# Kernel tuning notes

Measured on AMD Instinct MI355X. Metric: run time of the kernel, lower is better.

The kernel has to match this reference:

```python
import jax, jax.numpy as jnp
import numpy as np

B, F, D, H, E, K = 4, 2048, 1024, 2048, 8, 2  # batch, frames, dim, expert hidden, n_experts, top_k


def setup_inputs() -> dict:
    key = jax.random.key(0)
    ks = jax.random.split(key, 9)
    sc = lambda k, shape, fan_in: (jax.random.normal(k, shape, jnp.float32) * (fan_in ** -0.5))
    return {
        "x": jax.random.normal(ks[0], (B, F, D), jnp.float32),
        # router: Linear(D,D) -> SiLU -> Linear(D,E)
        "rw1": sc(ks[1], (D, D), D),
        "rb1": jnp.zeros((D,), jnp.float32),
        "rw2": sc(ks[2], (D, E), D),
        "rb2": jnp.zeros((E,), jnp.float32),
        # experts: E x (Linear(D,H) -> SiLU -> Linear(H,D))
        "ew1": sc(ks[3], (E, D, H), D),
        "eb1": jnp.zeros((E, H), jnp.float32),
        "ew2": sc(ks[4], (E, H, D), H),
        "eb2": jnp.zeros((E, D), jnp.float32),
    }


def reference(x, rw1, rb1, rw2, rb2, ew1, eb1, ew2, eb2):
    b, f, d = x.shape
    t = x.reshape(b * f, d)                                   # [T, D]
    # router (eval mode: no topk noise)
    logits = jax.nn.silu(t @ rw1 + rb1) @ rw2 + rb2            # [T, E]
    vals, idx = jax.lax.top_k(logits, K)                       # [T, K]
    rows = jnp.arange(t.shape[0])[:, None]
    masked = jnp.full_like(logits, -jnp.inf).at[rows, idx].set(vals)
    w = jax.nn.softmax(masked, axis=1)                         # [T, E], nonzero only on top-k
    # dense per-expert FFN, then weighted combine (residual: y starts as x)
    eh = jax.nn.silu(jnp.einsum('td,edh->teh', t, ew1) + eb1[None])   # [T, E, H]
    eo = jnp.einsum('teh,ehd->ted', eh, ew2) + eb2[None]              # [T, E, D]
    y = t + jnp.einsum('te,ted->td', w, eo)
    return y.reshape(b, f, d)
```

## Files before the change

kernel.cpp:

```cpp
#include <hip/hip_runtime.h>
#include <hip/hip_bf16.h>
#include <cstdint>
#include <cstddef>

#define T_TOK 8192
#define DDIM  1024
#define HDIM  2048
#define NEXP  8
#define TOPK  2
#define KAUG  (3 * DDIM)

typedef short bf16x8 __attribute__((ext_vector_type(8)));
typedef float f32x4  __attribute__((ext_vector_type(4)));

__device__ __forceinline__ unsigned short f2bf(float f) {
  union { float f; unsigned u; } v; v.f = f;
  unsigned r = v.u + 0x7FFFu + ((v.u >> 16) & 1u);
  return (unsigned short)(r >> 16);
}
__device__ __forceinline__ float bf2f(unsigned short h) {
  union { unsigned u; float f; } v; v.u = ((unsigned)h) << 16;
  return v.f;
}
__device__ __forceinline__ float silu_fast(float v) {
  return v / (1.0f + __expf(-v));
}
__device__ __forceinline__ float silu_precise(float v) {
  return v / (1.0f + expf(-v));
}

__device__ __forceinline__ void gload16(const unsigned short* g, unsigned short* l) {
  __builtin_amdgcn_global_load_lds(
      (const __attribute__((address_space(1))) unsigned int*)g,
      (__attribute__((address_space(3))) unsigned int*)l,
      16, 0, 0);
}

__global__ void split_x_kernel(const float* __restrict__ in,
                               unsigned short* __restrict__ xaug, int n4) {
  int i = blockIdx.x * blockDim.x + threadIdx.x;
  if (i >= n4) return;
  float4 v = ((const float4*)in)[i];
  int t = i / (DDIM / 4);
  int kc = (i % (DDIM / 4)) * 4;
  float f[4] = {v.x, v.y, v.z, v.w};
  ushort4 hi, lo;
  unsigned short h[4], l[4];
#pragma unroll
  for (int j = 0; j < 4; j++) {
    h[j] = f2bf(f[j]);
    l[j] = f2bf(f[j] - bf2f(h[j]));
  }
  hi.x = h[0]; hi.y = h[1]; hi.z = h[2]; hi.w = h[3];
  lo.x = l[0]; lo.y = l[1]; lo.z = l[2]; lo.w = l[3];
  *(ushort4*)&xaug[(size_t)t * KAUG + kc] = hi;
  *(ushort4*)&xaug[(size_t)t * KAUG + DDIM + kc] = hi;
  *(ushort4*)&xaug[(size_t)t * KAUG + 2 * DDIM + kc] = lo;
}

__global__ __launch_bounds__(256) void split_w_kernel(
    const float* __restrict__ in, unsigned short* __restrict__ waug) {
  __shared__ float tile[32][33];
  int c0 = blockIdx.x * 32, r0 = blockIdx.y * 32;
  int tx = threadIdx.x & 31, ty = threadIdx.x >> 5;
#pragma unroll
  for (int i = 0; i < 32; i += 8)
    tile[ty + i][tx] = in[(size_t)(r0 + ty + i) * DDIM + (c0 + tx)];
  __syncthreads();
#pragma unroll
  for (int i = 0; i < 32; i += 8) {
    float v = tile[tx][ty + i];
    unsigned short h = f2bf(v);
    unsigned short l = f2bf(v - bf2f(h));
    int n = c0 + ty + i, k = r0 + tx;
    waug[(size_t)n * KAUG + k] = h;
    waug[(size_t)n * KAUG + DDIM + k] = l;
    waug[(size_t)n * KAUG + 2 * DDIM + k] = h;
  }
}

__global__ __launch_bounds__(256) void transpose_conv_kernel(
    const float* __restrict__ in, unsigned short* __restrict__ out, int R, int C) {
  __shared__ float tile[32][33];
  const int z = blockIdx.z;
  const float* src = in + (size_t)z * R * C;
  unsigned short* dst = out + (size_t)z * R * C;
  int c0 = blockIdx.x * 32, r0 = blockIdx.y * 32;
  int tx = threadIdx.x & 31, ty = threadIdx.x >> 5;
#pragma unroll
  for (int i = 0; i < 32; i += 8)
    tile[ty + i][tx] = src[(size_t)(r0 + ty + i) * C + (c0 + tx)];
  __syncthreads();
#pragma unroll
  for (int i = 0; i < 32; i += 8)
    dst[(size_t)(c0 + ty + i) * R + (r0 + tx)] = f2bf(tile[tx][ty + i]);
}

__global__ void zero_small_kernel(int* __restrict__ counts, int* __restrict__ cursors) {
  int i = threadIdx.x;
  if (i < NEXP) { counts[i] = 0; cursors[i] = 0; }
}

template <int EPI>
__global__ __launch_bounds__(512, 2) void gemm_mfma4(
    const unsigned short* __restrict__ Abase,
    const unsigned short* __restrict__ Btbase,
    const float* __restrict__ bias,
    float* __restrict__ outF,
    unsigned short* __restrict__ outBf,
    const int* __restrict__ toks,
    const int* __restrict__ offs, const int* __restrict__ cnts,
    int N, int KD, int Astride, int numE, int nTiles, int mCap) {
  constexpr int BUFB = 49152;
  extern __shared__ char sm[];

  const int id = blockIdx.x;
  const int e = id % numE;
  const int r = id / numE;
  const int n0 = (r % nTiles) * 256;
  const int mb = r / nTiles;

  int ne = T_TOK, off = 0;
  if (EPI != 0) { ne = cnts[e]; off = offs[e]; }

  const unsigned short* Bt = Btbase + (size_t)e * N * KD;
  const unsigned short* A = (EPI == 2) ? (Abase + (size_t)off * Astride) : Abase;

  const int tid = threadIdx.x;
  const int lane = tid & 63, wid = tid >> 6;
  const int l16 = lane & 15, quad = lane >> 4;
  const int wm = wid >> 2, wn = wid & 3;

  const int rStage = tid >> 3;
  const int cS8 = ((tid & 7) ^ (rStage & 7)) * 8;
  const int ldsW = wid << 10;

  const int NT = KD / 64;
  const int mStride = mCap * 128;

  const int sw = l16 & 7;
  const int cOff0 = (quad ^ sw) << 4;
  const int cOff1 = ((quad + 4) ^ sw) << 4;
  const int aFragB = (wm * 64 + l16) << 7;
  const int bFragB = 16384 + ((wn * 64 + l16) << 7);

  const unsigned short* bP[4];
#pragma unroll
  for (int p = 0; p < 4; p++)
    bP[p] = Bt + (size_t)(n0 + p * 64 + rStage) * KD + cS8;

  for (int m0 = mb * 128; m0 < ne; m0 += mStride) {
    const unsigned short* aP[2];
#pragma unroll
    for (int p = 0; p < 2; p++) {
      int row = m0 + p * 64 + rStage;
      int idx;
      if (EPI == 1) idx = toks[off + min(row, ne - 1)];
      else if (EPI == 2) idx = min(row, ne - 1);
      else idx = row;
      aP[p] = A + (size_t)idx * Astride + cS8;
    }

    f32x4 acc[4][4];
    const f32x4 zf = {0.f, 0.f, 0.f, 0.f};
#pragma unroll
    for (int mi = 0; mi < 4; mi++)
#pragma unroll
      for (int ni = 0; ni < 4; ni++) acc[mi][ni] = zf;

    auto stage = [&](int t, int b) {
      char* base = sm + b * BUFB + ldsW;
      gload16(aP[0] + t * 64, (unsigned short*)(base));
      gload16(aP[1] + t * 64, (unsigned short*)(base + 8192));
      gload16(bP[0] + t * 64, (unsigned short*)(base + 16384));
      gload16(bP[1] + t * 64, (unsigned short*)(base + 24576));
      gload16(bP[2] + t * 64, (unsigned short*)(base + 32768));
      gload16(bP[3] + t * 64, (unsigned short*)(base + 40960));
    };

    stage(0, 0);
    stage(1, 1);
    stage(2, 2);

    for (int t = 0; t < NT; ++t) {
      const char* base = sm + (t % 3) * BUFB;
      if (t + 2 < NT)      __builtin_amdgcn_s_waitcnt(0x0F70 | 12);
      else if (t + 1 < NT) __builtin_amdgcn_s_waitcnt(0x0F70 | 6);
      else                 __builtin_amdgcn_s_waitcnt(0x0F70);
      __builtin_amdgcn_s_barrier();
      __builtin_amdgcn_sched_barrier(0);

      bf16x8 av[4], bv[4];
#pragma unroll
      for (int mi = 0; mi < 4; mi++)
        av[mi] = *(const bf16x8*)(base + aFragB + (mi << 11) + cOff0);
#pragma unroll
      for (int ni = 0; ni < 4; ni++)
        bv[ni] = *(const bf16x8*)(base + bFragB + (ni << 11) + cOff0);
      __builtin_amdgcn_s_waitcnt(0xC07F);
      __builtin_amdgcn_sched_barrier(0);
      __builtin_amdgcn_s_setprio(1);
#pragma unroll
      for (int mi = 0; mi < 4; mi++)
#pragma unroll
        for (int ni = 0; ni < 4; ni++)
          acc[mi][ni] = __builtin_amdgcn_mfma_f32_16x16x32_bf16(
              av[mi], bv[ni], acc[mi][ni], 0, 0, 0);
      __builtin_amdgcn_s_setprio(0);
      __builtin_amdgcn_s_barrier();

#pragma unroll
      for (int mi = 0; mi < 4; mi++)
        av[mi] = *(const bf16x8*)(base + aFragB + (mi << 11) + cOff1);
#pragma unroll
      for (int ni = 0; ni < 4; ni++)
        bv[ni] = *(const bf16x8*)(base + bFragB + (ni << 11) + cOff1);
      __builtin_amdgcn_s_waitcnt(0xC07F);
      __builtin_amdgcn_s_barrier();
      __builtin_amdgcn_sched_barrier(0);
      if (t + 3 < NT) stage(t + 3, t % 3);
      __builtin_amdgcn_s_setprio(1);
#pragma unroll
      for (int mi = 0; mi < 4; mi++)
#pragma unroll
        for (int ni = 0; ni < 4; ni++)
          acc[mi][ni] = __builtin_amdgcn_mfma_f32_16x16x32_bf16(
              av[mi], bv[ni], acc[mi][ni], 0, 0, 0);
      __builtin_amdgcn_s_setprio(0);
    }

    float bv4[4];
#pragma unroll
    for (int ni = 0; ni < 4; ni++)
      bv4[ni] = bias[(size_t)e * N + n0 + wn * 64 + ni * 16 + l16];
#pragma unroll
    for (int mi = 0; mi < 4; mi++) {
      const int prow = m0 + wm * 64 + mi * 16 + quad * 4;
#pragma unroll
      for (int rr = 0; rr < 4; rr++) {
        const int p = prow + rr;
        if (EPI != 0 && p >= ne) continue;
#pragma unroll
        for (int ni = 0; ni < 4; ni++) {
          const int col = n0 + wn * 64 + ni * 16 + l16;
          float v = acc[mi][ni][rr] + bv4[ni];
          if (EPI == 0) {
            outF[(size_t)p * N + col] = silu_precise(v);
          } else if (EPI == 1) {
            outBf[(size_t)(off + p) * N + col] = f2bf(silu_fast(v));
          } else {
            outBf[(size_t)(off + p) * N + col] = f2bf(v);
          }
        }
      }
    }
  }
}

__global__ __launch_bounds__(256) void router2_kernel(
    const float* __restrict__ rh, const float* __restrict__ rw2,
    const float* __restrict__ rb2, float* __restrict__ logits) {
  int t = blockIdx.x * 4 + (threadIdx.x >> 6);
  int lane = threadIdx.x & 63;
  const float* row = rh + (size_t)t * DDIM;
  float acc[NEXP];
#pragma unroll
  for (int e = 0; e < NEXP; e++) acc[e] = 0.f;
  for (int k = lane; k < DDIM; k += 64) {
    float v = row[k];
    const float* w = rw2 + (size_t)k * NEXP;
#pragma unroll
    for (int e = 0; e < NEXP; e++) acc[e] += v * w[e];
  }
#pragma unroll
  for (int e = 0; e < NEXP; e++) {
#pragma unroll
    for (int off = 32; off > 0; off >>= 1) acc[e] += __shfl_xor(acc[e], off, 64);
  }
#pragma unroll
  for (int e = 0; e < NEXP; e++)
    if (lane == e) logits[(size_t)t * NEXP + e] = acc[e] + rb2[e];
}

__global__ void topk_kernel(const float* __restrict__ logits,
                            int* __restrict__ idx2, float* __restrict__ w2arr,
                            int* __restrict__ counts) {
  int t = blockIdx.x * blockDim.x + threadIdx.x;
  if (t >= T_TOK) return;
  float l[NEXP];
#pragma unroll
  for (int e = 0; e < NEXP; e++) l[e] = logits[(size_t)t * NEXP + e];
  int i1 = 0; float v1 = l[0];
#pragma unroll
  for (int e = 1; e < NEXP; e++)
    if (l[e] > v1) { v1 = l[e]; i1 = e; }
  int i2 = -1; float v2 = -3.4e38f;
#pragma unroll
  for (int e = 0; e < NEXP; e++)
    if (e != i1 && l[e] > v2) { v2 = l[e]; i2 = e; }
  float ex = expf(v2 - v1);
  float wa = 1.f / (1.f + ex);
  float wb = ex / (1.f + ex);
  idx2[t * 2] = i1; idx2[t * 2 + 1] = i2;
  w2arr[t * 2] = wa; w2arr[t * 2 + 1] = wb;
  atomicAdd(&counts[i1], 1);
  atomicAdd(&counts[i2], 1);
}

__global__ void prefix_kernel(const int* __restrict__ counts, int* __restrict__ offs) {
  if (threadIdx.x == 0 && blockIdx.x == 0) {
    int s = 0;
    for (int e = 0; e < NEXP; e++) { offs[e] = s; s += counts[e]; }
  }
}

__global__ void scatter_kernel(const int* __restrict__ idx2,
                               const int* __restrict__ offs, int* __restrict__ cursors,
                               int* __restrict__ toks, int* __restrict__ posArr) {
  int t = blockIdx.x * blockDim.x + threadIdx.x;
  if (t >= T_TOK) return;
#pragma unroll
  for (int j = 0; j < TOPK; j++) {
    int e = idx2[t * 2 + j];
    int pos = atomicAdd(&cursors[e], 1);
    int s = offs[e] + pos;
    toks[s] = t;
    posArr[t * 2 + j] = s;
  }
}

__global__ __launch_bounds__(256) void combine_kernel(
    const float* __restrict__ x, const unsigned short* __restrict__ eo,
    const int* __restrict__ posArr, const float* __restrict__ w2arr,
    float* __restrict__ y) {
  const int t = blockIdx.x;
  const int d = threadIdx.x * 4;
  const int s0 = posArr[t * 2], s1 = posArr[t * 2 + 1];
  const float w0 = w2arr[t * 2], w1 = w2arr[t * 2 + 1];
  float4 xv = *(const float4*)&x[(size_t)t * DDIM + d];
  ushort4 a = *(const ushort4*)&eo[(size_t)s0 * DDIM + d];
  ushort4 b = *(const ushort4*)&eo[(size_t)s1 * DDIM + d];
  float4 o;
  o.x = xv.x + w0 * bf2f(a.x) + w1 * bf2f(b.x);
  o.y = xv.y + w0 * bf2f(a.y) + w1 * bf2f(b.y);
  o.z = xv.z + w0 * bf2f(a.z) + w1 * bf2f(b.z);
  o.w = xv.w + w0 * bf2f(a.w) + w1 * bf2f(b.w);
  *(float4*)&y[(size_t)t * DDIM + d] = o;
}

extern "C" void kernel_launch(void* const* d_in, const int* in_sizes, int n_in,
                              void* d_out, int out_size, void* d_ws, size_t ws_size,
                              hipStream_t stream) {
  (void)in_sizes; (void)n_in; (void)out_size; (void)ws_size;
  const float* x   = (const float*)d_in[0];
  const float* rw1 = (const float*)d_in[1];
  const float* rb1 = (const float*)d_in[2];
  const float* rw2 = (const float*)d_in[3];
  const float* rb2 = (const float*)d_in[4];
  const float* ew1 = (const float*)d_in[5];
  const float* eb1 = (const float*)d_in[6];
  const float* ew2 = (const float*)d_in[7];
  const float* eb2 = (const float*)d_in[8];
  float* y = (float*)d_out;

  char* ws = (char*)d_ws;
  size_t o = 0;
  auto alloc = [&](size_t bytes) {
    size_t r = o;
    o += (bytes + 255) & ~(size_t)255;
    return r;
  };
  unsigned short* xaug  = (unsigned short*)(ws + alloc((size_t)T_TOK * KAUG * 2));
  unsigned short* waug  = (unsigned short*)(ws + alloc((size_t)DDIM * KAUG * 2));
  unsigned short* ew1t  = (unsigned short*)(ws + alloc((size_t)NEXP * HDIM * DDIM * 2));
  unsigned short* ew2t  = (unsigned short*)(ws + alloc((size_t)NEXP * DDIM * HDIM * 2));
  float*          rh    = (float*)(ws + alloc((size_t)T_TOK * DDIM * 4));
  float*          logits= (float*)(ws + alloc((size_t)T_TOK * NEXP * 4));
  int*            idx2  = (int*)(ws + alloc((size_t)T_TOK * 2 * 4));
  float*          w2    = (float*)(ws + alloc((size_t)T_TOK * 2 * 4));
  int*            toks  = (int*)(ws + alloc((size_t)T_TOK * TOPK * 4));
  int*            posArr= (int*)(ws + alloc((size_t)T_TOK * TOPK * 4));
  int*            counts= (int*)(ws + alloc(256));
  int*            cursors=(int*)(ws + alloc(256));
  int*            offs  = (int*)(ws + alloc(256));
  unsigned short* ehb   = (unsigned short*)(ws + alloc((size_t)T_TOK * TOPK * HDIM * 2));
  unsigned short* eo    = (unsigned short*)(ws + alloc((size_t)T_TOK * TOPK * DDIM * 2));

  constexpr int LDS_SZ = 3 * 49152;
  static bool s_attr = false;
  if (!s_attr) {
    (void)hipFuncSetAttribute((const void*)gemm_mfma4<0>,
                              hipFuncAttributeMaxDynamicSharedMemorySize, LDS_SZ);
    (void)hipFuncSetAttribute((const void*)gemm_mfma4<1>,
                              hipFuncAttributeMaxDynamicSharedMemorySize, LDS_SZ);
    (void)hipFuncSetAttribute((const void*)gemm_mfma4<2>,
                              hipFuncAttributeMaxDynamicSharedMemorySize, LDS_SZ);
    s_attr = true;
  }

  zero_small_kernel<<<1, 64, 0, stream>>>(counts, cursors);

  const int n4 = T_TOK * DDIM / 4;
  split_x_kernel<<<(n4 + 255) / 256, 256, 0, stream>>>(x, xaug, n4);
  split_w_kernel<<<dim3(DDIM / 32, DDIM / 32), 256, 0, stream>>>(rw1, waug);
  transpose_conv_kernel<<<dim3(HDIM / 32, DDIM / 32, NEXP), 256, 0, stream>>>(ew1, ew1t, DDIM, HDIM);
  transpose_conv_kernel<<<dim3(DDIM / 32, HDIM / 32, NEXP), 256, 0, stream>>>(ew2, ew2t, HDIM, DDIM);

  gemm_mfma4<0><<<256, 512, LDS_SZ, stream>>>(
      xaug, waug, rb1, rh, nullptr, nullptr, nullptr, nullptr,
      DDIM, KAUG, KAUG, 1, 4, 64);
  router2_kernel<<<T_TOK / 4, 256, 0, stream>>>(rh, rw2, rb2, logits);
  topk_kernel<<<T_TOK / 256, 256, 0, stream>>>(logits, idx2, w2, counts);
  prefix_kernel<<<1, 64, 0, stream>>>(counts, offs);
  scatter_kernel<<<T_TOK / 256, 256, 0, stream>>>(idx2, offs, cursors, toks, posArr);

  gemm_mfma4<1><<<8 * 8 * 16, 512, LDS_SZ, stream>>>(
      xaug, ew1t, eb1, nullptr, ehb, toks, offs, counts,
      HDIM, DDIM, KAUG, NEXP, 8, 16);
  gemm_mfma4<2><<<8 * 4 * 16, 512, LDS_SZ, stream>>>(
      ehb, ew2t, eb2, nullptr, eo, nullptr, offs, counts,
      DDIM, HDIM, HDIM, NEXP, 4, 16);
  combine_kernel<<<T_TOK, 256, 0, stream>>>(x, eo, posArr, w2, y);
}
```

Baseline: 747.6 us.

## Enlarge GEMM tile to 256x256 with double-buffered quarter-staged ping-pong pipeline

Rewrites the shared MFMA GEMM so each 512-thread block computes a 256x256 output tile instead of 128x256, doubling the per-wave accumulators to 8x4. The triple-buffered LDS pipeline becomes a double buffer, and A and B halves are staged separately between four MFMA phases so loads interleave with compute. The goal is more arithmetic per byte moved through LDS and global memory. In exchange, grids shrink (128, 256 and 256 blocks), register pressure rises, and wasted padding grows for experts whose token count is not a multiple of 256.

Result: no change. 742.0 us (-0.8%).

```diff
diff --git a/kernel.cpp b/kernel.cpp
--- a/kernel.cpp
+++ b/kernel.cpp
@@ -102,7 +102,7 @@
 }
 
 template <int EPI>
-__global__ __launch_bounds__(512, 2) void gemm_mfma4(
+__global__ __launch_bounds__(512, 2) void gemm8p(
     const unsigned short* __restrict__ Abase,
     const unsigned short* __restrict__ Btbase,
     const float* __restrict__ bias,
@@ -111,7 +111,6 @@
     const int* __restrict__ toks,
     const int* __restrict__ offs, const int* __restrict__ cnts,
     int N, int KD, int Astride, int numE, int nTiles, int mCap) {
-  constexpr int BUFB = 49152;
   extern __shared__ char sm[];
 
   const int id = blockIdx.x;
@@ -136,23 +135,23 @@
   const int ldsW = wid << 10;
 
   const int NT = KD / 64;
-  const int mStride = mCap * 128;
+  const int mStride = mCap * 256;
 
   const int sw = l16 & 7;
   const int cOff0 = (quad ^ sw) << 4;
   const int cOff1 = ((quad + 4) ^ sw) << 4;
-  const int aFragB = (wm * 64 + l16) << 7;
-  const int bFragB = 16384 + ((wn * 64 + l16) << 7);
+  const int aRowB = (wm * 128 + l16) << 7;
+  const int bRowB = (wn * 64 + l16) << 7;
 
   const unsigned short* bP[4];
 #pragma unroll
   for (int p = 0; p < 4; p++)
     bP[p] = Bt + (size_t)(n0 + p * 64 + rStage) * KD + cS8;
 
-  for (int m0 = mb * 128; m0 < ne; m0 += mStride) {
-    const unsigned short* aP[2];
-#pragma unroll
-    for (int p = 0; p < 2; p++) {
+  for (int m0 = mb * 256; m0 < ne; m0 += mStride) {
+    const unsigned short* aP[4];
+#pragma unroll
+    for (int p = 0; p < 4; p++) {
       int row = m0 + p * 64 + rStage;
       int idx;
       if (EPI == 1) idx = toks[off + min(row, ne - 1)];
@@ -161,72 +160,125 @@
       aP[p] = A + (size_t)idx * Astride + cS8;
     }
 
-    f32x4 acc[4][4];
+    auto stA0 = [&](int t) { char* b = sm + (t & 1) * 32768 + ldsW; int kb = t * 64;
+      gload16(aP[0] + kb, (unsigned short*)b);
+      gload16(aP[1] + kb, (unsigned short*)(b + 8192)); };
+    auto stA1 = [&](int t) { char* b = sm + (t & 1) * 32768 + 16384 + ldsW; int kb = t * 64;
+      gload16(aP[2] + kb, (unsigned short*)b);
+      gload16(aP[3] + kb, (unsigned short*)(b + 8192)); };
+    auto stB0 = [&](int t) { char* b = sm + 65536 + (t & 1) * 32768 + ldsW; int kb = t * 64;
+      gload16(bP[0] + kb, (unsigned short*)b);
+      gload16(bP[1] + kb, (unsigned short*)(b + 8192)); };
+    auto stB1 = [&](int t) { char* b = sm + 65536 + (t & 1) * 32768 + 16384 + ldsW; int kb = t * 64;
+      gload16(bP[2] + kb, (unsigned short*)b);
+      gload16(bP[3] + kb, (unsigned short*)(b + 8192)); };
+
+    f32x4 acc[8][4];
     const f32x4 zf = {0.f, 0.f, 0.f, 0.f};
 #pragma unroll
-    for (int mi = 0; mi < 4; mi++)
+    for (int mi = 0; mi < 8; mi++)
 #pragma unroll
       for (int ni = 0; ni < 4; ni++) acc[mi][ni] = zf;
 
-    auto stage = [&](int t, int b) {
-      char* base = sm + b * BUFB + ldsW;
-      gload16(aP[0] + t * 64, (unsigned short*)(base));
-      gload16(aP[1] + t * 64, (unsigned short*)(base + 8192));
-      gload16(bP[0] + t * 64, (unsigned short*)(base + 16384));
-      gload16(bP[1] + t * 64, (unsigned short*)(base + 24576));
-      gload16(bP[2] + t * 64, (unsigned short*)(base + 32768));
-      gload16(bP[3] + t * 64, (unsigned short*)(base + 40960));
-    };
-
-    stage(0, 0);
-    stage(1, 1);
-    stage(2, 2);
+    stA0(0); stB0(0); stA1(0); stB1(0);
+    __builtin_amdgcn_s_waitcnt(0x0F74);
+    stA0(1); stB0(1); stA1(1);
+    __builtin_amdgcn_s_waitcnt(0x0F76);
+    __builtin_amdgcn_s_barrier();
 
     for (int t = 0; t < NT; ++t) {
-      const char* base = sm + (t % 3) * BUFB;
-      if (t + 2 < NT)      __builtin_amdgcn_s_waitcnt(0x0F70 | 12);
-      else if (t + 1 < NT) __builtin_amdgcn_s_waitcnt(0x0F70 | 6);
-      else                 __builtin_amdgcn_s_waitcnt(0x0F70);
-      __builtin_amdgcn_s_barrier();
-      __builtin_amdgcn_sched_barrier(0);
-
-      bf16x8 av[4], bv[4];
-#pragma unroll
-      for (int mi = 0; mi < 4; mi++)
-        av[mi] = *(const bf16x8*)(base + aFragB + (mi << 11) + cOff0);
-#pragma unroll
-      for (int ni = 0; ni < 4; ni++)
-        bv[ni] = *(const bf16x8*)(base + bFragB + (ni << 11) + cOff0);
+      const char* bA = sm + (t & 1) * 32768;
+      const char* bB = bA + 65536;
+      bf16x8 aR[8], bR0[4], bR1[4];
+
+#pragma unroll
+      for (int mi = 0; mi < 4; mi++) {
+        aR[mi * 2]     = *(const bf16x8*)(bA + aRowB + mi * 2048 + cOff0);
+        aR[mi * 2 + 1] = *(const bf16x8*)(bA + aRowB + mi * 2048 + cOff1);
+      }
+#pragma unroll
+      for (int ni = 0; ni < 2; ni++) {
+        bR0[ni * 2]     = *(const bf16x8*)(bB + bRowB + ni * 2048 + cOff0);
+        bR0[ni * 2 + 1] = *(const bf16x8*)(bB + bRowB + ni * 2048 + cOff1);
+      }
+      if (t + 1 < NT) stB1(t + 1);
+      __builtin_amdgcn_s_waitcnt(0xC87F);
+      __builtin_amdgcn_s_barrier();
       __builtin_amdgcn_s_waitcnt(0xC07F);
       __builtin_amdgcn_sched_barrier(0);
       __builtin_amdgcn_s_setprio(1);
 #pragma unroll
       for (int mi = 0; mi < 4; mi++)
 #pragma unroll
-        for (int ni = 0; ni < 4; ni++)
+        for (int ni = 0; ni < 2; ni++) {
           acc[mi][ni] = __builtin_amdgcn_mfma_f32_16x16x32_bf16(
-              av[mi], bv[ni], acc[mi][ni], 0, 0, 0);
+              aR[mi * 2], bR0[ni * 2], acc[mi][ni], 0, 0, 0);
+          acc[mi][ni] = __builtin_amdgcn_mfma_f32_16x16x32_bf16(
+              aR[mi * 2 + 1], bR0[ni * 2 + 1], acc[mi][ni], 0, 0, 0);
+        }
       __builtin_amdgcn_s_setprio(0);
       __builtin_amdgcn_s_barrier();
 
 #pragma unroll
+      for (int ni = 0; ni < 2; ni++) {
+        bR1[ni * 2]     = *(const bf16x8*)(bB + bRowB + (ni + 2) * 2048 + cOff0);
+        bR1[ni * 2 + 1] = *(const bf16x8*)(bB + bRowB + (ni + 2) * 2048 + cOff1);
+      }
+      __builtin_amdgcn_s_barrier();
+      __builtin_amdgcn_s_waitcnt(0xC07F);
+      __builtin_amdgcn_sched_barrier(0);
+      __builtin_amdgcn_s_setprio(1);
+#pragma unroll
       for (int mi = 0; mi < 4; mi++)
-        av[mi] = *(const bf16x8*)(base + aFragB + (mi << 11) + cOff1);
-#pragma unroll
-      for (int ni = 0; ni < 4; ni++)
-        bv[ni] = *(const bf16x8*)(base + bFragB + (ni << 11) + cOff1);
+#pragma unroll
+        for (int ni = 0; ni < 2; ni++) {
+          acc[mi][ni + 2] = __builtin_amdgcn_mfma_f32_16x16x32_bf16(
+              aR[mi * 2], bR1[ni * 2], acc[mi][ni + 2], 0, 0, 0);
+          acc[mi][ni + 2] = __builtin_amdgcn_mfma_f32_16x16x32_bf16(
+              aR[mi * 2 + 1], bR1[ni * 2 + 1], acc[mi][ni + 2], 0, 0, 0);
+        }
+      __builtin_amdgcn_s_setprio(0);
+      __builtin_amdgcn_s_barrier();
+
+#pragma unroll
+      for (int mi = 0; mi < 4; mi++) {
+        aR[mi * 2]     = *(const bf16x8*)(bA + aRowB + (mi + 4) * 2048 + cOff0);
+        aR[mi * 2 + 1] = *(const bf16x8*)(bA + aRowB + (mi + 4) * 2048 + cOff1);
+      }
+      if (t + 2 < NT) stB0(t + 2);
+      __builtin_amdgcn_s_barrier();
       __builtin_amdgcn_s_waitcnt(0xC07F);
-      __builtin_amdgcn_s_barrier();
       __builtin_amdgcn_sched_barrier(0);
-      if (t + 3 < NT) stage(t + 3, t % 3);
       __builtin_amdgcn_s_setprio(1);
 #pragma unroll
       for (int mi = 0; mi < 4; mi++)
 #pragma unroll
-        for (int ni = 0; ni < 4; ni++)
-          acc[mi][ni] = __builtin_amdgcn_mfma_f32_16x16x32_bf16(
-              av[mi], bv[ni], acc[mi][ni], 0, 0, 0);
+        for (int ni = 0; ni < 2; ni++) {
+          acc[mi + 4][ni + 2] = __builtin_amdgcn_mfma_f32_16x16x32_bf16(
+              aR[mi * 2], bR1[ni * 2], acc[mi + 4][ni + 2], 0, 0, 0);
+          acc[mi + 4][ni + 2] = __builtin_amdgcn_mfma_f32_16x16x32_bf16(
+              aR[mi * 2 + 1], bR1[ni * 2 + 1], acc[mi + 4][ni + 2], 0, 0, 0);
+        }
       __builtin_amdgcn_s_setprio(0);
+      __builtin_amdgcn_s_barrier();
+
+      if (t + 2 < NT) { stA0(t + 2); stA1(t + 2); }
+      __builtin_amdgcn_s_barrier();
+      __builtin_amdgcn_sched_barrier(0);
+      __builtin_amdgcn_s_setprio(1);
+#pragma unroll
+      for (int mi = 0; mi < 4; mi++)
+#pragma unroll
+        for (int ni = 0; ni < 2; ni++) {
+          acc[mi + 4][ni] = __builtin_amdgcn_mfma_f32_16x16x32_bf16(
+              aR[mi * 2], bR0[ni * 2], acc[mi + 4][ni], 0, 0, 0);
+          acc[mi + 4][ni] = __builtin_amdgcn_mfma_f32_16x16x32_bf16(
+              aR[mi * 2 + 1], bR0[ni * 2 + 1], acc[mi + 4][ni], 0, 0, 0);
+        }
+      __builtin_amdgcn_s_setprio(0);
+      if (t + 2 < NT)      __builtin_amdgcn_s_waitcnt(0x0F76);
+      else if (t + 1 < NT) __builtin_amdgcn_s_waitcnt(0x0F70);
+      __builtin_amdgcn_s_barrier();
     }
 
     float bv4[4];
@@ -234,8 +286,8 @@
     for (int ni = 0; ni < 4; ni++)
       bv4[ni] = bias[(size_t)e * N + n0 + wn * 64 + ni * 16 + l16];
 #pragma unroll
-    for (int mi = 0; mi < 4; mi++) {
-      const int prow = m0 + wm * 64 + mi * 16 + quad * 4;
+    for (int mi = 0; mi < 8; mi++) {
+      const int prow = m0 + wm * 128 + mi * 16 + quad * 4;
 #pragma unroll
       for (int rr = 0; rr < 4; rr++) {
         const int p = prow + rr;
@@ -386,14 +438,14 @@
   unsigned short* ehb   = (unsigned short*)(ws + alloc((size_t)T_TOK * TOPK * HDIM * 2));
   unsigned short* eo    = (unsigned short*)(ws + alloc((size_t)T_TOK * TOPK * DDIM * 2));
 
-  constexpr int LDS_SZ = 3 * 49152;
+  constexpr int LDS_SZ = 131072;
   static bool s_attr = false;
   if (!s_attr) {
-    (void)hipFuncSetAttribute((const void*)gemm_mfma4<0>,
+    (void)hipFuncSetAttribute((const void*)gemm8p<0>,
                               hipFuncAttributeMaxDynamicSharedMemorySize, LDS_SZ);
-    (void)hipFuncSetAttribute((const void*)gemm_mfma4<1>,
+    (void)hipFuncSetAttribute((const void*)gemm8p<1>,
                               hipFuncAttributeMaxDynamicSharedMemorySize, LDS_SZ);
-    (void)hipFuncSetAttribute((const void*)gemm_mfma4<2>,
+    (void)hipFuncSetAttribute((const void*)gemm8p<2>,
                               hipFuncAttributeMaxDynamicSharedMemorySize, LDS_SZ);
     s_attr = true;
   }
@@ -406,19 +458,19 @@
   transpose_conv_kernel<<<dim3(HDIM / 32, DDIM / 32, NEXP), 256, 0, stream>>>(ew1, ew1t, DDIM, HDIM);
   transpose_conv_kernel<<<dim3(DDIM / 32, HDIM / 32, NEXP), 256, 0, stream>>>(ew2, ew2t, HDIM, DDIM);
 
-  gemm_mfma4<0><<<256, 512, LDS_SZ, stream>>>(
+  gemm8p<0><<<128, 512, LDS_SZ, stream>>>(
       xaug, waug, rb1, rh, nullptr, nullptr, nullptr, nullptr,
-      DDIM, KAUG, KAUG, 1, 4, 64);
+      DDIM, KAUG, KAUG, 1, 4, 32);
   router2_kernel<<<T_TOK / 4, 256, 0, stream>>>(rh, rw2, rb2, logits);
   topk_kernel<<<T_TOK / 256, 256, 0, stream>>>(logits, idx2, w2, counts);
   prefix_kernel<<<1, 64, 0, stream>>>(counts, offs);
   scatter_kernel<<<T_TOK / 256, 256, 0, stream>>>(idx2, offs, cursors, toks, posArr);
 
-  gemm_mfma4<1><<<8 * 8 * 16, 512, LDS_SZ, stream>>>(
+  gemm8p<1><<<8 * 8 * 4, 512, LDS_SZ, stream>>>(
       xaug, ew1t, eb1, nullptr, ehb, toks, offs, counts,
-      HDIM, DDIM, KAUG, NEXP, 8, 16);
-  gemm_mfma4<2><<<8 * 4 * 16, 512, LDS_SZ, stream>>>(
+      HDIM, DDIM, KAUG, NEXP, 8, 4);
+  gemm8p<2><<<8 * 4 * 8, 512, LDS_SZ, stream>>>(
       ehb, ew2t, eb2, nullptr, eo, nullptr, offs, counts,
-      DDIM, HDIM, HDIM, NEXP, 4, 16);
+      DDIM, HDIM, HDIM, NEXP, 4, 8);
   combine_kernel<<<T_TOK, 256, 0, stream>>>(x, eo, posArr, w2, y);
 }
```

## Shrink GEMM tiles to 128x128 with 256 threads and double buffering

Applied to the files above, without the earlier changes.

Replaces the 512-thread, 128x256-tile GEMM with a 256-thread, 128x128-tile version. The LDS pipeline drops from three stages to two (64 KB instead of 144 KB), and the next stage is prefetched at the top of each k-step. Grids double in size to cover the narrower N tiles. The aim is higher occupancy and more blocks per CU. The cost is less operand reuse per tile and a shallower prefetch that may expose global-load latency.

After: 694.1 us. -7.2%, faster.

```diff
diff --git a/kernel.cpp b/kernel.cpp
--- a/kernel.cpp
+++ b/kernel.cpp
@@ -102,7 +102,7 @@
 }
 
 template <int EPI>
-__global__ __launch_bounds__(512, 2) void gemm_mfma4(
+__global__ __launch_bounds__(256) void gemm_s(
     const unsigned short* __restrict__ Abase,
     const unsigned short* __restrict__ Btbase,
     const float* __restrict__ bias,
@@ -111,13 +111,12 @@
     const int* __restrict__ toks,
     const int* __restrict__ offs, const int* __restrict__ cnts,
     int N, int KD, int Astride, int numE, int nTiles, int mCap) {
-  constexpr int BUFB = 49152;
   extern __shared__ char sm[];
 
   const int id = blockIdx.x;
   const int e = id % numE;
   const int r = id / numE;
-  const int n0 = (r % nTiles) * 256;
+  const int n0 = (r % nTiles) * 128;
   const int mb = r / nTiles;
 
   int ne = T_TOK, off = 0;
@@ -129,7 +128,7 @@
   const int tid = threadIdx.x;
   const int lane = tid & 63, wid = tid >> 6;
   const int l16 = lane & 15, quad = lane >> 4;
-  const int wm = wid >> 2, wn = wid & 3;
+  const int wm = wid >> 1, wn = wid & 1;
 
   const int rStage = tid >> 3;
   const int cS8 = ((tid & 7) ^ (rStage & 7)) * 8;
@@ -141,19 +140,19 @@
   const int sw = l16 & 7;
   const int cOff0 = (quad ^ sw) << 4;
   const int cOff1 = ((quad + 4) ^ sw) << 4;
-  const int aFragB = (wm * 64 + l16) << 7;
-  const int bFragB = 16384 + ((wn * 64 + l16) << 7);
+  const int aRowB = (wm * 64 + l16) << 7;
+  const int bRowB = 16384 + ((wn * 64 + l16) << 7);
 
   const unsigned short* bP[4];
 #pragma unroll
   for (int p = 0; p < 4; p++)
-    bP[p] = Bt + (size_t)(n0 + p * 64 + rStage) * KD + cS8;
+    bP[p] = Bt + (size_t)(n0 + p * 32 + rStage) * KD + cS8;
 
   for (int m0 = mb * 128; m0 < ne; m0 += mStride) {
-    const unsigned short* aP[2];
-#pragma unroll
-    for (int p = 0; p < 2; p++) {
-      int row = m0 + p * 64 + rStage;
+    const unsigned short* aP[4];
+#pragma unroll
+    for (int p = 0; p < 4; p++) {
+      int row = m0 + p * 32 + rStage;
       int idx;
       if (EPI == 1) idx = toks[off + min(row, ne - 1)];
       else if (EPI == 2) idx = min(row, ne - 1);
@@ -169,36 +168,48 @@
       for (int ni = 0; ni < 4; ni++) acc[mi][ni] = zf;
 
     auto stage = [&](int t, int b) {
-      char* base = sm + b * BUFB + ldsW;
-      gload16(aP[0] + t * 64, (unsigned short*)(base));
-      gload16(aP[1] + t * 64, (unsigned short*)(base + 8192));
-      gload16(bP[0] + t * 64, (unsigned short*)(base + 16384));
-      gload16(bP[1] + t * 64, (unsigned short*)(base + 24576));
-      gload16(bP[2] + t * 64, (unsigned short*)(base + 32768));
-      gload16(bP[3] + t * 64, (unsigned short*)(base + 40960));
+      char* base = sm + b * 32768 + ldsW;
+      const int kb = t * 64;
+#pragma unroll
+      for (int p = 0; p < 4; p++) {
+        gload16(aP[p] + kb, (unsigned short*)(base + p * 4096));
+        gload16(bP[p] + kb, (unsigned short*)(base + 16384 + p * 4096));
+      }
     };
 
     stage(0, 0);
-    stage(1, 1);
-    stage(2, 2);
 
     for (int t = 0; t < NT; ++t) {
-      const char* base = sm + (t % 3) * BUFB;
-      if (t + 2 < NT)      __builtin_amdgcn_s_waitcnt(0x0F70 | 12);
-      else if (t + 1 < NT) __builtin_amdgcn_s_waitcnt(0x0F70 | 6);
-      else                 __builtin_amdgcn_s_waitcnt(0x0F70);
+      if (t + 1 < NT) {
+        stage(t + 1, (t + 1) & 1);
+        __builtin_amdgcn_s_waitcnt(0x0F78);
+      } else {
+        __builtin_amdgcn_s_waitcnt(0x0F70);
+      }
       __builtin_amdgcn_s_barrier();
-      __builtin_amdgcn_sched_barrier(0);
-
+
+      const char* base = sm + (t & 1) * 32768;
       bf16x8 av[4], bv[4];
 #pragma unroll
       for (int mi = 0; mi < 4; mi++)
-        av[mi] = *(const bf16x8*)(base + aFragB + (mi << 11) + cOff0);
+        av[mi] = *(const bf16x8*)(base + aRowB + mi * 2048 + cOff0);
 #pragma unroll
       for (int ni = 0; ni < 4; ni++)
-        bv[ni] = *(const bf16x8*)(base + bFragB + (ni << 11) + cOff0);
-      __builtin_amdgcn_s_waitcnt(0xC07F);
-      __builtin_amdgcn_sched_barrier(0);
+        bv[ni] = *(const bf16x8*)(base + bRowB + ni * 2048 + cOff0);
+      __builtin_amdgcn_s_setprio(1);
+#pragma unroll
+      for (int mi = 0; mi < 4; mi++)
+#pragma unroll
+        for (int ni = 0; ni < 4; ni++)
+          acc[mi][ni] = __builtin_amdgcn_mfma_f32_16x16x32_bf16(
+              av[mi], bv[ni], acc[mi][ni], 0, 0, 0);
+      __builtin_amdgcn_s_setprio(0);
+#pragma unroll
+      for (int mi = 0; mi < 4; mi++)
+        av[mi] = *(const bf16x8*)(base + aRowB + mi * 2048 + cOff1);
+#pragma unroll
+      for (int ni = 0; ni < 4; ni++)
+        bv[ni] = *(const bf16x8*)(base + bRowB + ni * 2048 + cOff1);
       __builtin_amdgcn_s_setprio(1);
 #pragma unroll
       for (int mi = 0; mi < 4; mi++)
@@ -208,25 +219,6 @@
               av[mi], bv[ni], acc[mi][ni], 0, 0, 0);
       __builtin_amdgcn_s_setprio(0);
       __builtin_amdgcn_s_barrier();
-
-#pragma unroll
-      for (int mi = 0; mi < 4; mi++)
-        av[mi] = *(const bf16x8*)(base + aFragB + (mi << 11) + cOff1);
-#pragma unroll
-      for (int ni = 0; ni < 4; ni++)
-        bv[ni] = *(const bf16x8*)(base + bFragB + (ni << 11) + cOff1);
-      __builtin_amdgcn_s_waitcnt(0xC07F);
-      __builtin_amdgcn_s_barrier();
-      __builtin_amdgcn_sched_barrier(0);
-      if (t + 3 < NT) stage(t + 3, t % 3);
-      __builtin_amdgcn_s_setprio(1);
-#pragma unroll
-      for (int mi = 0; mi < 4; mi++)
-#pragma unroll
-        for (int ni = 0; ni < 4; ni++)
-          acc[mi][ni] = __builtin_amdgcn_mfma_f32_16x16x32_bf16(
-              av[mi], bv[ni], acc[mi][ni], 0, 0, 0);
-      __builtin_amdgcn_s_setprio(0);
     }
 
     float bv4[4];
@@ -386,14 +378,14 @@
   unsigned short* ehb   = (unsigned short*)(ws + alloc((size_t)T_TOK * TOPK * HDIM * 2));
   unsigned short* eo    = (unsigned short*)(ws + alloc((size_t)T_TOK * TOPK * DDIM * 2));
 
-  constexpr int LDS_SZ = 3 * 49152;
+  constexpr int LDS_SZ = 65536;
   static bool s_attr = false;
   if (!s_attr) {
-    (void)hipFuncSetAttribute((const void*)gemm_mfma4<0>,
+    (void)hipFuncSetAttribute((const void*)gemm_s<0>,
                               hipFuncAttributeMaxDynamicSharedMemorySize, LDS_SZ);
-    (void)hipFuncSetAttribute((const void*)gemm_mfma4<1>,
+    (void)hipFuncSetAttribute((const void*)gemm_s<1>,
                               hipFuncAttributeMaxDynamicSharedMemorySize, LDS_SZ);
-    (void)hipFuncSetAttribute((const void*)gemm_mfma4<2>,
+    (void)hipFuncSetAttribute((const void*)gemm_s<2>,
                               hipFuncAttributeMaxDynamicSharedMemorySize, LDS_SZ);
     s_attr = true;
   }
@@ -406,19 +398,19 @@
   transpose_conv_kernel<<<dim3(HDIM / 32, DDIM / 32, NEXP), 256, 0, stream>>>(ew1, ew1t, DDIM, HDIM);
   transpose_conv_kernel<<<dim3(DDIM / 32, HDIM / 32, NEXP), 256, 0, stream>>>(ew2, ew2t, HDIM, DDIM);
 
-  gemm_mfma4<0><<<256, 512, LDS_SZ, stream>>>(
+  gemm_s<0><<<512, 256, LDS_SZ, stream>>>(
       xaug, waug, rb1, rh, nullptr, nullptr, nullptr, nullptr,
-      DDIM, KAUG, KAUG, 1, 4, 64);
+      DDIM, KAUG, KAUG, 1, 8, 64);
   router2_kernel<<<T_TOK / 4, 256, 0, stream>>>(rh, rw2, rb2, logits);
   topk_kernel<<<T_TOK / 256, 256, 0, stream>>>(logits, idx2, w2, counts);
   prefix_kernel<<<1, 64, 0, stream>>>(counts, offs);
   scatter_kernel<<<T_TOK / 256, 256, 0, stream>>>(idx2, offs, cursors, toks, posArr);
 
-  gemm_mfma4<1><<<8 * 8 * 16, 512, LDS_SZ, stream>>>(
+  gemm_s<1><<<8 * 16 * 16, 256, LDS_SZ, stream>>>(
       xaug, ew1t, eb1, nullptr, ehb, toks, offs, counts,
-      HDIM, DDIM, KAUG, NEXP, 8, 16);
-  gemm_mfma4<2><<<8 * 4 * 16, 512, LDS_SZ, stream>>>(
+      HDIM, DDIM, KAUG, NEXP, 16, 16);
+  gemm_s<2><<<8 * 8 * 16, 256, LDS_SZ, stream>>>(
       ehb, ew2t, eb2, nullptr, eo, nullptr, offs, counts,
-      DDIM, HDIM, HDIM, NEXP, 4, 16);
+      DDIM, HDIM, HDIM, NEXP, 8, 16);
   combine_kernel<<<T_TOK, 256, 0, stream>>>(x, eo, posArr, w2, y);
 }
```
